# Optimization experiments

Measured on AMD Instinct MI355X. Metric: run time of the kernel, lower is better.

## Reference

```python
import jax, jax.numpy as jnp
import numpy as np


def _to_complex(x):
    # trailing axis holds (real, imag)
    return x[..., 0] + 1j * x[..., 1]


def _nufft2c(img, omega, csm):
    """Exact type-2 non-uniform DFT with coil sensitivities (reference for nufft2c_torch).

    img:   (H, W) real or complex image
    omega: (2, M) k-space coords in cycles/pixel, in [-0.5, 0.5]
    csm:   (C, H, W) complex coil sensitivity maps
    returns (C, M) complex k-space, centered & orthonormal-style 1/sqrt(HW) scaling.
    """
    H, W = img.shape
    y = jnp.arange(H, dtype=jnp.float32) - H / 2.0  # centered pixel coords
    z = jnp.arange(W, dtype=jnp.float32) - W / 2.0
    ey = jnp.exp(-2j * jnp.pi * omega[0][:, None] * y[None, :])  # (M, H)
    ez = jnp.exp(-2j * jnp.pi * omega[1][:, None] * z[None, :])  # (M, W)
    sim = csm * img[None, :, :].astype(csm.dtype)                # (C, H, W)
    tmp = jnp.einsum('chw,mw->cmh', sim, ez)                     # (C, M, H)
    k = jnp.einsum('cmh,mh->cm', tmp, ey) / np.float32(np.sqrt(H * W))
    return k


def setup_inputs() -> dict:
    key = jax.random.key(0)
    k0, k1, k2, k3, k4 = jax.random.split(key, 5)
    H = W = 300
    C = 4       # coils
    M = 4096    # non-Cartesian k-space samples
    img_pred = jax.random.normal(k0, (H, W, 1), jnp.float32)
    kdata = jax.random.normal(k1, (1, C, M, 2), jnp.float32)
    all_omega = jax.random.uniform(k2, (1, 2, M), jnp.float32) - 0.5  # cycles/pixel
    all_dcomp = jax.random.uniform(k3, (1, M), jnp.float32)
    all_csm = jax.random.normal(k4, (C, H, W, 2), jnp.float32)
    return {
        'img_pred': img_pred,
        'kdata': kdata,
        'all_omega': all_omega,
        'all_dcomp': all_dcomp,
        'all_csm': all_csm,
    }


def reference(img_pred, kdata, all_omega, all_dcomp, all_csm):
    Ncontrast = 1
    csm = _to_complex(all_csm)   # (C, H, W)
    kd = _to_complex(kdata)      # (Ncontrast, C, M)
    two_pi = jnp.float32(2.0 * np.pi)
    # radial k-space weighting, (Ncontrast, M)
    weight = jnp.sqrt((all_omega[:, 0, :] * two_pi) ** 2 +
                      (all_omega[:, 1, :] * two_pi) ** 2) + 1.0
    loss = jnp.float32(0.0)
    for ii in range(Ncontrast):
        img = img_pred[:, :, ii]                       # (H, W)
        ksp = _nufft2c(img, all_omega[ii], csm)        # (C, M)
        d = weight[ii][None, :] * (ksp - kd[ii])       # weighted complex residual
        # MSELoss over view_as_real == mean over all real & imag components
        loss = loss + jnp.mean(jnp.stack([d.real, d.imag]) ** 2)
    return loss
```

## Files before the change

### kernel.cpp

```cpp
#include <hip/hip_runtime.h>
#include <math.h>

#define HH 300
#define WW 300
#define CC 4
#define MM 4096
#define KP 640
#define CSTRIDE 384
#define MP (CC*CSTRIDE)
#define NP 8192
#define BK 128
#define NRB (MP/128)

typedef __attribute__((ext_vector_type(4))) float f32x4;
typedef __attribute__((ext_vector_type(4))) int int4v;
typedef __attribute__((ext_vector_type(8))) int int8v;
typedef const __attribute__((address_space(1))) void g_void;
typedef __attribute__((address_space(3))) void l_void;

#define TWO_PI 6.283185307179586f

__device__ __forceinline__ float aval(const float* img, const float* csm,
                                      int c, int h, int k) {
    if (k >= 2 * WW) return 0.0f;
    int w = (k < WW) ? k : k - WW;
    float im = img[h * WW + w];
    const float* cs = csm + (((size_t)c * HH + h) * WW + w) * 2;
    return ((k < WW) ? cs[0] : cs[1]) * im;
}

__global__ __launch_bounds__(256) void prep_kernel(
    const float* __restrict__ img, const float* __restrict__ csm,
    const float* __restrict__ omega, ushort* __restrict__ A,
    unsigned char* __restrict__ B, float* __restrict__ out)
{
    const int bid = blockIdx.x;
    if (bid == 0 && threadIdx.x == 0) out[0] = 0.0f;
    const int ABLK = (MP * KP / 2) / 256;
    if (bid < ABLK) {
        int idx = bid * 256 + threadIdx.x;
        int row = idx / (KP / 2);
        int k   = (idx - row * (KP / 2)) * 2;
        int c = row / CSTRIDE;
        int h = row - c * CSTRIDE;
        float v0 = 0.0f, v1 = 0.0f;
        if (h < HH) { v0 = aval(img, csm, c, h, k); v1 = aval(img, csm, c, h, k + 1); }
        int pk = __builtin_amdgcn_cvt_pk_fp8_f32(v0, v1, 0, false);
        A[idx] = (ushort)pk;
    } else {
        int idx = (bid - ABLK) * 256 + threadIdx.x;
        int m  = idx / 160;
        int wp = idx - m * 160;
        unsigned char* r0 = B + (size_t)m * KP;
        unsigned char* r1 = B + (size_t)(m + MM) * KP;
        if (wp < 150) {
            int w = wp * 2;
            float om1 = omega[MM + m];
            float s0, c0, s1, c1;
            __sincosf(TWO_PI * om1 * (float)(w - 150), &s0, &c0);
            __sincosf(TWO_PI * om1 * (float)(w - 149), &s1, &c1);
            ushort rr = (ushort)__builtin_amdgcn_cvt_pk_fp8_f32(c0, c1, 0, false);
            ushort ii = (ushort)__builtin_amdgcn_cvt_pk_fp8_f32(-s0, -s1, 0, false);
            ushort ni = (ushort)__builtin_amdgcn_cvt_pk_fp8_f32(s0, s1, 0, false);
            *(ushort*)(r0 + w)       = rr;
            *(ushort*)(r0 + WW + w)  = ni;
            *(ushort*)(r1 + w)       = ii;
            *(ushort*)(r1 + WW + w)  = rr;
        } else {
            int z = (wp - 150) * 4;
            *(unsigned int*)(r0 + 600 + z) = 0u;
            *(unsigned int*)(r1 + 600 + z) = 0u;
        }
    }
}

__global__ __launch_bounds__(256) void gemm_kernel(
    const unsigned char* __restrict__ A, const unsigned char* __restrict__ B,
    const float* __restrict__ omega, float2* __restrict__ P)
{
    __shared__ unsigned char As[128 * BK];
    __shared__ unsigned char Bs[128 * BK];
    __shared__ float2 red[128];

    const int t    = threadIdx.x;
    const int wave = t >> 6;
    const int ln   = t & 63;
    const int row0 = blockIdx.y * 128;
    const int col0 = blockIdx.x * 128;
    const int wr = wave >> 1, wc = wave & 1;
    const int lr = ln & 15;
    const int lq = ln >> 4;

    if (t < 128) red[t] = make_float2(0.0f, 0.0f);

    const int srow  = t >> 3;
    const int cphys = (t >> 1) & 3;
    const int half  = t & 1;
    const int sgoff = ((cphys ^ (srow & 3)) << 5) + (half << 4);

    f32x4 acc[4][4] = {};

    for (int k0 = 0; k0 < KP; k0 += BK) {
        #pragma unroll
        for (int p = 0; p < 4; ++p) {
            const unsigned char* gA = A + (size_t)(row0 + p * 32 + srow) * KP + k0 + sgoff;
            const unsigned char* gB = B + (size_t)(col0 + p * 32 + srow) * KP + k0 + sgoff;
            __builtin_amdgcn_global_load_lds((g_void*)gA, (l_void*)(As + p * 4096 + t * 16), 16, 0, 0);
            __builtin_amdgcn_global_load_lds((g_void*)gB, (l_void*)(Bs + p * 4096 + t * 16), 16, 0, 0);
        }
        __syncthreads();

        int8v a[4], b[4];
        #pragma unroll
        for (int i = 0; i < 4; ++i) {
            const int r = wr * 64 + i * 16 + lr;
            const unsigned char* pA = As + r * BK + ((lq ^ (lr & 3)) << 5);
            int4v lo = *(const int4v*)pA;
            int4v hi = *(const int4v*)(pA + 16);
            a[i] = __builtin_shufflevector(lo, hi, 0, 1, 2, 3, 4, 5, 6, 7);
        }
        #pragma unroll
        for (int j = 0; j < 4; ++j) {
            const int r = wc * 64 + j * 16 + lr;
            const unsigned char* pB = Bs + r * BK + ((lq ^ (lr & 3)) << 5);
            int4v lo = *(const int4v*)pB;
            int4v hi = *(const int4v*)(pB + 16);
            b[j] = __builtin_shufflevector(lo, hi, 0, 1, 2, 3, 4, 5, 6, 7);
        }
        #pragma unroll
        for (int i = 0; i < 4; ++i)
            #pragma unroll
            for (int j = 0; j < 4; ++j)
                acc[i][j] = __builtin_amdgcn_mfma_scale_f32_16x16x128_f8f6f4(
                    a[i], b[j], acc[i][j], 0, 0,
                    0, 0x7f7f7f7f, 0, 0x7f7f7f7f);
        __syncthreads();
    }

    const int c  = row0 / CSTRIDE;
    const int h0 = row0 - c * CSTRIDE;

    #pragma unroll
    for (int j = 0; j < 4; ++j) {
        const int jcol = wc * 64 + j * 16 + lr;
        const int m = (col0 + jcol) & (MM - 1);
        const float om0 = omega[m];
        float ss, sc;
        __sincosf(TWO_PI * om0, &ss, &sc);
        const float str = sc, sti = -ss;
        float s2r = str * str - sti * sti, s2i = 2.0f * str * sti;
        float s4r = s2r * s2r - s2i * s2i, s4i = 2.0f * s2r * s2i;
        float s8r = s4r * s4r - s4i * s4i, s8i = 2.0f * s4r * s4i;
        float s16r = s8r * s8r - s8i * s8i, s16i = 2.0f * s8r * s8i;

        const int hb0 = h0 + wr * 64 + lq * 4;
        float sn, cs;
        __sincosf(TWO_PI * om0 * (float)(hb0 - 150), &sn, &cs);
        float byr = cs, byi = -sn;

        float pr = 0.0f, pi = 0.0f;
        #pragma unroll
        for (int i = 0; i < 4; ++i) {
            float er = byr, ei = byi;
            #pragma unroll
            for (int r = 0; r < 4; ++r) {
                const float v = acc[i][j][r];
                pr = fmaf(v, er, pr);
                pi = fmaf(v, ei, pi);
                float nr = er * str - ei * sti;
                ei = er * sti + ei * str;
                er = nr;
            }
            float nbr = byr * s16r - byi * s16i;
            byi = byr * s16i + byi * s16r;
            byr = nbr;
        }
        pr += __shfl_down(pr, 32); pi += __shfl_down(pi, 32);
        pr += __shfl_down(pr, 16); pi += __shfl_down(pi, 16);
        if (lq == 0) {
            atomicAdd(&red[jcol].x, pr);
            atomicAdd(&red[jcol].y, pi);
        }
    }
    __syncthreads();

    if (t < 128) {
        const int rb = row0 >> 7;
        P[(size_t)rb * NP + col0 + t] = red[t];
    }
}

__global__ __launch_bounds__(64) void loss_kernel(
    const float2* __restrict__ P, const float* __restrict__ kdata,
    const float* __restrict__ omega, float* __restrict__ out)
{
    const int t = blockIdx.x * 64 + threadIdx.x;
    const int c = t >> 12;
    const int m = t & (MM - 1);

    float kr = 0.0f, ki = 0.0f;
    #pragma unroll
    for (int q = 0; q < 3; ++q) {
        const int rb = 3 * c + q;
        float2 p0 = P[(size_t)rb * NP + m];
        float2 p1 = P[(size_t)rb * NP + m + MM];
        kr += p0.x - p1.y;
        ki += p0.y + p1.x;
    }
    kr *= (1.0f / 300.0f);
    ki *= (1.0f / 300.0f);

    const float om0 = omega[m];
    const float om1 = omega[MM + m];
    const size_t kidx = ((size_t)c * MM + m) * 2;
    const float kdr = kdata[kidx];
    const float kdi = kdata[kidx + 1];
    const float w0 = om0 * TWO_PI, w1 = om1 * TWO_PI;
    const float wg = sqrtf(w0 * w0 + w1 * w1) + 1.0f;
    const float dr = wg * (kr - kdr);
    const float di = wg * (ki - kdi);
    float val = (dr * dr + di * di) * (1.0f / (2.0f * CC * MM));

    #pragma unroll
    for (int off = 32; off > 0; off >>= 1) val += __shfl_down(val, off);
    if (threadIdx.x == 0) atomicAdd(out, val);
}

extern "C" void kernel_launch(void* const* d_in, const int* in_sizes, int n_in,
                              void* d_out, int out_size, void* d_ws, size_t ws_size,
                              hipStream_t stream) {
    const float* img   = (const float*)d_in[0];
    const float* kdata = (const float*)d_in[1];
    const float* omega = (const float*)d_in[2];
    const float* csm   = (const float*)d_in[4];
    float* out = (float*)d_out;

    unsigned char* Aws = (unsigned char*)d_ws;
    unsigned char* Bws = (unsigned char*)d_ws + (1u << 20);
    float2*        Pws = (float2*)((char*)d_ws + (8u << 20));

    const int ablk = (MP * KP / 2) / 256;
    const int bblk = (MM * 160) / 256;
    prep_kernel<<<ablk + bblk, 256, 0, stream>>>(img, csm, omega,
                                                 (ushort*)Aws, Bws, out);
    gemm_kernel<<<dim3(NP / 128, MP / 128), 256, 0, stream>>>(Aws, Bws, omega, Pws);
    loss_kernel<<<CC * MM / 64, 64, 0, stream>>>(Pws, kdata, omega, out);
}
```

Measured before the change: 89.77 us.

## Store GEMM operands in k-chunked layout and load MFMA fragments directly from global

The prep kernel now writes A and B in a 32-byte k-chunk-major layout, so each MFMA lane's 32-byte fragment is contiguous and neighbouring rows are adjacent. The GEMM drops LDS staging, the swizzle and the per-iteration barriers, and loads operand fragments straight from global memory in a fully unrolled k loop. This removes LDS traffic and synchronisation, but reuse across waves now depends on the L1/L2 caches instead of shared memory, and the prep writes become strided.

```diff
diff --git a/kernel.cpp b/kernel.cpp
--- a/kernel.cpp
+++ b/kernel.cpp
@@ -6,19 +6,21 @@
 #define CC 4
 #define MM 4096
 #define KP 640
+#define NKC (KP/32)
 #define CSTRIDE 384
 #define MP (CC*CSTRIDE)
 #define NP 8192
-#define BK 128
 #define NRB (MP/128)
 
 typedef __attribute__((ext_vector_type(4))) float f32x4;
 typedef __attribute__((ext_vector_type(4))) int int4v;
 typedef __attribute__((ext_vector_type(8))) int int8v;
-typedef const __attribute__((address_space(1))) void g_void;
-typedef __attribute__((address_space(3))) void l_void;
 
 #define TWO_PI 6.283185307179586f
+
+__device__ __forceinline__ size_t cmaddr(int R, int row, int k) {
+    return ((size_t)(k >> 5) * R + row) * 32 + (k & 31);
+}
 
 __device__ __forceinline__ float aval(const float* img, const float* csm,
                                       int c, int h, int k) {
@@ -31,7 +33,7 @@
 
 __global__ __launch_bounds__(256) void prep_kernel(
     const float* __restrict__ img, const float* __restrict__ csm,
-    const float* __restrict__ omega, ushort* __restrict__ A,
+    const float* __restrict__ omega, unsigned char* __restrict__ A,
     unsigned char* __restrict__ B, float* __restrict__ out)
 {
     const int bid = blockIdx.x;
@@ -46,13 +48,11 @@
         float v0 = 0.0f, v1 = 0.0f;
         if (h < HH) { v0 = aval(img, csm, c, h, k); v1 = aval(img, csm, c, h, k + 1); }
         int pk = __builtin_amdgcn_cvt_pk_fp8_f32(v0, v1, 0, false);
-        A[idx] = (ushort)pk;
+        *(ushort*)(A + cmaddr(MP, row, k)) = (ushort)pk;
     } else {
         int idx = (bid - ABLK) * 256 + threadIdx.x;
         int m  = idx / 160;
         int wp = idx - m * 160;
-        unsigned char* r0 = B + (size_t)m * KP;
-        unsigned char* r1 = B + (size_t)(m + MM) * KP;
         if (wp < 150) {
             int w = wp * 2;
             float om1 = omega[MM + m];
@@ -62,14 +62,14 @@
             ushort rr = (ushort)__builtin_amdgcn_cvt_pk_fp8_f32(c0, c1, 0, false);
             ushort ii = (ushort)__builtin_amdgcn_cvt_pk_fp8_f32(-s0, -s1, 0, false);
             ushort ni = (ushort)__builtin_amdgcn_cvt_pk_fp8_f32(s0, s1, 0, false);
-            *(ushort*)(r0 + w)       = rr;
-            *(ushort*)(r0 + WW + w)  = ni;
-            *(ushort*)(r1 + w)       = ii;
-            *(ushort*)(r1 + WW + w)  = rr;
+            *(ushort*)(B + cmaddr(NP, m,      w))        = rr;
+            *(ushort*)(B + cmaddr(NP, m,      WW + w))   = ni;
+            *(ushort*)(B + cmaddr(NP, m + MM, w))        = ii;
+            *(ushort*)(B + cmaddr(NP, m + MM, WW + w))   = rr;
         } else {
-            int z = (wp - 150) * 4;
-            *(unsigned int*)(r0 + 600 + z) = 0u;
-            *(unsigned int*)(r1 + 600 + z) = 0u;
+            int k = 600 + (wp - 150) * 4;
+            *(unsigned int*)(B + cmaddr(NP, m,      k)) = 0u;
+            *(unsigned int*)(B + cmaddr(NP, m + MM, k)) = 0u;
         }
     }
 }
@@ -78,8 +78,6 @@
     const unsigned char* __restrict__ A, const unsigned char* __restrict__ B,
     const float* __restrict__ omega, float2* __restrict__ P)
 {
-    __shared__ unsigned char As[128 * BK];
-    __shared__ unsigned char Bs[128 * BK];
     __shared__ float2 red[128];
 
     const int t    = threadIdx.x;
@@ -93,36 +91,24 @@
 
     if (t < 128) red[t] = make_float2(0.0f, 0.0f);
 
-    const int srow  = t >> 3;
-    const int cphys = (t >> 1) & 3;
-    const int half  = t & 1;
-    const int sgoff = ((cphys ^ (srow & 3)) << 5) + (half << 4);
+    const int arow = row0 + wr * 64 + lr;
+    const int bcol = col0 + wc * 64 + lr;
 
     f32x4 acc[4][4] = {};
 
-    for (int k0 = 0; k0 < KP; k0 += BK) {
-        #pragma unroll
-        for (int p = 0; p < 4; ++p) {
-            const unsigned char* gA = A + (size_t)(row0 + p * 32 + srow) * KP + k0 + sgoff;
-            const unsigned char* gB = B + (size_t)(col0 + p * 32 + srow) * KP + k0 + sgoff;
-            __builtin_amdgcn_global_load_lds((g_void*)gA, (l_void*)(As + p * 4096 + t * 16), 16, 0, 0);
-            __builtin_amdgcn_global_load_lds((g_void*)gB, (l_void*)(Bs + p * 4096 + t * 16), 16, 0, 0);
-        }
-        __syncthreads();
-
+    #pragma unroll
+    for (int kc = 0; kc < NKC; kc += 4) {
         int8v a[4], b[4];
         #pragma unroll
         for (int i = 0; i < 4; ++i) {
-            const int r = wr * 64 + i * 16 + lr;
-            const unsigned char* pA = As + r * BK + ((lq ^ (lr & 3)) << 5);
+            const unsigned char* pA = A + ((size_t)(kc + lq) * MP + arow + i * 16) * 32;
             int4v lo = *(const int4v*)pA;
             int4v hi = *(const int4v*)(pA + 16);
             a[i] = __builtin_shufflevector(lo, hi, 0, 1, 2, 3, 4, 5, 6, 7);
         }
         #pragma unroll
         for (int j = 0; j < 4; ++j) {
-            const int r = wc * 64 + j * 16 + lr;
-            const unsigned char* pB = Bs + r * BK + ((lq ^ (lr & 3)) << 5);
+            const unsigned char* pB = B + ((size_t)(kc + lq) * NP + bcol + j * 16) * 32;
             int4v lo = *(const int4v*)pB;
             int4v hi = *(const int4v*)(pB + 16);
             b[j] = __builtin_shufflevector(lo, hi, 0, 1, 2, 3, 4, 5, 6, 7);
@@ -134,8 +120,9 @@
                 acc[i][j] = __builtin_amdgcn_mfma_scale_f32_16x16x128_f8f6f4(
                     a[i], b[j], acc[i][j], 0, 0,
                     0, 0x7f7f7f7f, 0, 0x7f7f7f7f);
-        __syncthreads();
-    }
+    }
+
+    __syncthreads();
 
     const int c  = row0 / CSTRIDE;
     const int h0 = row0 - c * CSTRIDE;
@@ -241,8 +228,7 @@
 
     const int ablk = (MP * KP / 2) / 256;
     const int bblk = (MM * 160) / 256;
-    prep_kernel<<<ablk + bblk, 256, 0, stream>>>(img, csm, omega,
-                                                 (ushort*)Aws, Bws, out);
+    prep_kernel<<<ablk + bblk, 256, 0, stream>>>(img, csm, omega, Aws, Bws, out);
     gemm_kernel<<<dim3(NP / 128, MP / 128), 256, 0, stream>>>(Aws, Bws, omega, Pws);
     loss_kernel<<<CC * MM / 64, 64, 0, stream>>>(Pws, kdata, omega, out);
 }
```

Result: faster. 84.02 us (-6.4%).
